# Kernel optimization log

Measured on AMD Instinct MI355X. Metric: run time of the kernel, lower is better.

The kernel has to match this reference:

```python
import jax, jax.numpy as jnp
import numpy as np

N = 50000      # nodes
E = 800000     # edges (before self-loops)
IN = 128       # in_channels
C = 64         # hidden_channels
HD = 4         # heads
SLOPE = 0.2    # GATConv leaky_relu negative slope
EPS_BN = 1e-5


def add_self_loops(edge_index, n):
    loop = jnp.arange(n, dtype=edge_index.dtype)
    return jnp.concatenate([edge_index, jnp.stack([loop, loop])], axis=1)


def gat_conv(x, edge_index, W, a_src, a_dst, bias, heads, out_c, concat, n):
    src, dst = edge_index[0], edge_index[1]
    h = (x @ W).reshape(n, heads, out_c)                 # [N,H,C]
    al_s = jnp.sum(h * a_src, axis=-1)                   # [N,H]
    al_d = jnp.sum(h * a_dst, axis=-1)                   # [N,H]
    e = jax.nn.leaky_relu(al_s[src] + al_d[dst], SLOPE)  # [Etot,H]
    m = jax.ops.segment_max(e, dst, num_segments=n)      # segment softmax (stable)
    ex = jnp.exp(e - m[dst])
    s = jax.ops.segment_sum(ex, dst, num_segments=n)
    alpha = ex / (s[dst] + 1e-16)                        # [Etot,H]
    out = jax.ops.segment_sum(h[src] * alpha[:, :, None], dst, num_segments=n)
    out = out.reshape(n, heads * out_c) if concat else out.mean(axis=1)
    return out + bias


def batch_norm(x, gamma, beta):
    mu = x.mean(axis=0)
    var = x.var(axis=0)
    return (x - mu) * jax.lax.rsqrt(var + EPS_BN) * gamma + beta


def setup_inputs() -> dict:
    key = jax.random.key(0)
    ks = jax.random.split(key, 24)
    f = lambda k, shp, sc: (jax.random.normal(k, shp, dtype=jnp.float32) * sc)
    HC = HD * C
    return {
        "x": f(ks[0], (N, IN), 1.0),
        "edge_index": jax.random.randint(ks[1], (2, E), 0, N, dtype=jnp.int64),
        # conv1: IN -> C, heads=HD, concat
        "W1": f(ks[2], (IN, HC), 0.05), "as1": f(ks[3], (HD, C), 0.05),
        "ad1": f(ks[4], (HD, C), 0.05), "b1": f(ks[5], (HC,), 0.02),
        "g1": jnp.ones((HC,), jnp.float32), "bb1": jnp.zeros((HC,), jnp.float32),
        # conv2: HC -> C, heads=HD, concat
        "W2": f(ks[6], (HC, HC), 0.05), "as2": f(ks[7], (HD, C), 0.05),
        "ad2": f(ks[8], (HD, C), 0.05), "b2": f(ks[9], (HC,), 0.02),
        "g2": jnp.ones((HC,), jnp.float32), "bb2": jnp.zeros((HC,), jnp.float32),
        # conv3: HC -> C, heads=1, mean
        "W3": f(ks[10], (HC, C), 0.05), "as3": f(ks[11], (1, C), 0.05),
        "ad3": f(ks[12], (1, C), 0.05), "b3": f(ks[13], (C,), 0.02),
        # skips
        "Ws1": f(ks[14], (IN, HC), 0.05), "bs1": f(ks[15], (HC,), 0.02),
        "Ws2": f(ks[16], (HC, C), 0.05), "bs2": f(ks[17], (C,), 0.02),
    }


def reference(x, edge_index, W1, as1, ad1, b1, g1, bb1,
              W2, as2, ad2, b2, g2, bb2,
              W3, as3, ad3, b3, Ws1, bs1, Ws2, bs2):
    ei = add_self_loops(edge_index, N)
    x_init = x @ Ws1 + bs1
    h = gat_conv(x, ei, W1, as1, ad1, b1, HD, C, True, N)
    h = jax.nn.elu(batch_norm(h, g1, bb1)) + x_init
    x_skip = h @ Ws2 + bs2
    h = gat_conv(h, ei, W2, as2, ad2, b2, HD, C, True, N)
    h = jax.nn.elu(batch_norm(h, g2, bb2))
    out = gat_conv(h, ei, W3, as3, ad3, b3, 1, C, False, N) + x_skip
    return out
```

## Files before the change

kernel.cpp:

```cpp
#include <hip/hip_runtime.h>
#include <hip/hip_bf16.h>
#include <cstdint>
#include <cstddef>


#define LRELU_SLOPE 0.2f

typedef __attribute__((ext_vector_type(8))) short short8;
typedef __attribute__((ext_vector_type(4))) float f32x4;

__device__ __forceinline__ float bf2f(unsigned short u) {
  union { unsigned int i; float f; } t; t.i = ((unsigned int)u) << 16; return t.f;
}
__device__ __forceinline__ unsigned short f2bf(float f) {
  __hip_bfloat16 h = __float2bfloat16(f);
  return *reinterpret_cast<unsigned short*>(&h);
}

template<int K, int WAVES_GAT, int WAVES_SKIP>
__global__ __launch_bounds__((WAVES_GAT + WAVES_SKIP) * 64)
void gemm_gat_fused(const unsigned short* __restrict__ A,
                    const unsigned short* __restrict__ BtH,
                    const unsigned short* __restrict__ BtS,
                    const float* __restrict__ a_s, const float* __restrict__ a_d,
                    const float* __restrict__ biasS,
                    unsigned short* __restrict__ Hout,
                    float* __restrict__ als, float* __restrict__ ald,
                    unsigned short* __restrict__ Sout, int M) {
  constexpr int NKS = K / 32;
  constexpr int NH  = WAVES_GAT * 64;
  constexpr int NS  = WAVES_SKIP * 64;
  const int wid  = threadIdx.x >> 6;
  const int lane = threadIdx.x & 63;
  const int r    = lane & 15;
  const int q    = lane >> 4;
  const int koff = q * 8;
  const bool isGat = wid < WAVES_GAT;
  const int colbase = isGat ? wid * 64 : (wid - WAVES_GAT) * 64;
  const unsigned short* Bt = isGat ? BtH : BtS;

  short8 b[4][NKS];
  #pragma unroll
  for (int nf = 0; nf < 4; ++nf)
    #pragma unroll
    for (int ks = 0; ks < NKS; ++ks)
      b[nf][ks] = *(const short8*)(Bt + (size_t)(colbase + nf * 16 + r) * K + ks * 32 + koff);

  float as4[4] = {}, ad4[4] = {};
  if (isGat) {
    #pragma unroll
    for (int nf = 0; nf < 4; ++nf) {
      as4[nf] = a_s[colbase + nf * 16 + r];
      ad4[nf] = a_d[colbase + nf * 16 + r];
    }
  }

  const int ntiles = (M + 15) >> 4;
  const int chunk = (ntiles + 7) >> 3;
  const int xcd   = blockIdx.x & 7;
  const int lo    = xcd * chunk;
  const int hi    = min(lo + chunk, ntiles);
  const int bstep = gridDim.x >> 3;
  for (int t = lo + (blockIdx.x >> 3); t < hi; t += bstep) {
    const int row = t * 16 + r;
    short8 a[NKS];
    #pragma unroll
    for (int ks = 0; ks < NKS; ++ks) {
      a[ks] = (short8)(short)0;
      if (row < M) a[ks] = *(const short8*)(A + (size_t)row * K + ks * 32 + koff);
    }
    f32x4 acc[4];
    #pragma unroll
    for (int nf = 0; nf < 4; ++nf) acc[nf] = (f32x4)0.0f;
    #pragma unroll
    for (int ks = 0; ks < NKS; ++ks)
      #pragma unroll
      for (int nf = 0; nf < 4; ++nf)
        acc[nf] = __builtin_amdgcn_mfma_f32_16x16x32_bf16(a[ks], b[nf][ks], acc[nf], 0, 0, 0);

    const int rbase = t * 16 + q * 4;
    if (isGat) {
      #pragma unroll
      for (int nf = 0; nf < 4; ++nf) {
        const int col = colbase + nf * 16 + r;
        #pragma unroll
        for (int i = 0; i < 4; ++i) {
          const int rr = rbase + i;
          if (rr < M) Hout[(size_t)rr * NH + col] = f2bf(acc[nf][i]);
        }
      }
      #pragma unroll
      for (int i = 0; i < 4; ++i) {
        float s = 0.f, d = 0.f;
        #pragma unroll
        for (int nf = 0; nf < 4; ++nf) {
          s = fmaf(acc[nf][i], as4[nf], s);
          d = fmaf(acc[nf][i], ad4[nf], d);
        }
        #pragma unroll
        for (int m = 8; m >= 1; m >>= 1) {
          s += __shfl_xor(s, m, 64);
          d += __shfl_xor(d, m, 64);
        }
        const int rr = rbase + i;
        if (r == 0 && rr < M) {
          als[(size_t)rr * WAVES_GAT + wid] = s;
          ald[(size_t)rr * WAVES_GAT + wid] = d;
        }
      }
    } else {
      #pragma unroll
      for (int nf = 0; nf < 4; ++nf) {
        const int col = colbase + nf * 16 + r;
        const float bs = biasS[col];
        #pragma unroll
        for (int i = 0; i < 4; ++i) {
          const int rr = rbase + i;
          if (rr < M) Sout[(size_t)rr * NS + col] = f2bf(acc[nf][i] + bs);
        }
      }
    }
  }
}

__global__ __launch_bounds__(256)
void gemm_gat3(const unsigned short* __restrict__ A, const unsigned short* __restrict__ Bt,
               const float* __restrict__ a_s, const float* __restrict__ a_d,
               unsigned short* __restrict__ Hout, float* __restrict__ als,
               float* __restrict__ ald, int M) {
  constexpr int K = 256, NKS = 8;
  const int wid  = threadIdx.x >> 6;
  const int lane = threadIdx.x & 63;
  const int r    = lane & 15;
  const int q    = lane >> 4;
  const int koff = q * 8;

  short8 b[4][NKS];
  #pragma unroll
  for (int nf = 0; nf < 4; ++nf)
    #pragma unroll
    for (int ks = 0; ks < NKS; ++ks)
      b[nf][ks] = *(const short8*)(Bt + (size_t)(nf * 16 + r) * K + ks * 32 + koff);
  float as4[4], ad4[4];
  #pragma unroll
  for (int nf = 0; nf < 4; ++nf) {
    as4[nf] = a_s[nf * 16 + r];
    ad4[nf] = a_d[nf * 16 + r];
  }

  const int ntiles = (M + 15) >> 4;
  const int chunk = (ntiles + 7) >> 3;
  const int xcd   = blockIdx.x & 7;
  const int lo    = xcd * chunk;
  const int hi    = min(lo + chunk, ntiles);
  const int bstep = (gridDim.x >> 3) * 4;
  for (int t = lo + (blockIdx.x >> 3) * 4 + wid; t < hi; t += bstep) {
    const int row = t * 16 + r;
    short8 a[NKS];
    #pragma unroll
    for (int ks = 0; ks < NKS; ++ks) {
      a[ks] = (short8)(short)0;
      if (row < M) a[ks] = *(const short8*)(A + (size_t)row * K + ks * 32 + koff);
    }
    f32x4 acc[4];
    #pragma unroll
    for (int nf = 0; nf < 4; ++nf) acc[nf] = (f32x4)0.0f;
    #pragma unroll
    for (int ks = 0; ks < NKS; ++ks)
      #pragma unroll
      for (int nf = 0; nf < 4; ++nf)
        acc[nf] = __builtin_amdgcn_mfma_f32_16x16x32_bf16(a[ks], b[nf][ks], acc[nf], 0, 0, 0);

    const int rbase = t * 16 + q * 4;
    #pragma unroll
    for (int nf = 0; nf < 4; ++nf) {
      const int col = nf * 16 + r;
      #pragma unroll
      for (int i = 0; i < 4; ++i) {
        const int rr = rbase + i;
        if (rr < M) Hout[(size_t)rr * 64 + col] = f2bf(acc[nf][i]);
      }
    }
    #pragma unroll
    for (int i = 0; i < 4; ++i) {
      float s = 0.f, d = 0.f;
      #pragma unroll
      for (int nf = 0; nf < 4; ++nf) {
        s = fmaf(acc[nf][i], as4[nf], s);
        d = fmaf(acc[nf][i], ad4[nf], d);
      }
      #pragma unroll
      for (int m = 8; m >= 1; m >>= 1) {
        s += __shfl_xor(s, m, 64);
        d += __shfl_xor(d, m, 64);
      }
      const int rr = rbase + i;
      if (r == 0 && rr < M) { als[rr] = s; ald[rr] = d; }
    }
  }
}

__global__ __launch_bounds__(256)
void prep_all(const float* __restrict__ x,
              const float* __restrict__ W1, const float* __restrict__ Ws1,
              const float* __restrict__ W2, const float* __restrict__ Ws2,
              const float* __restrict__ W3,
              unsigned short* __restrict__ xb,
              unsigned short* __restrict__ W1t, unsigned short* __restrict__ Ws1t,
              unsigned short* __restrict__ W2t, unsigned short* __restrict__ Ws2t,
              unsigned short* __restrict__ W3t, int n) {
  int idx = blockIdx.x * blockDim.x + threadIdx.x;
  const int nx = n * 32;
  if (idx < nx) {
    float4 v = ((const float4*)x)[idx];
    ushort4 o;
    o.x = f2bf(v.x); o.y = f2bf(v.y); o.z = f2bf(v.z); o.w = f2bf(v.w);
    ((ushort4*)xb)[idx] = o;
    return;
  }
  idx -= nx;
  if (idx < 256 * 128) { int nn = idx >> 7, kk = idx & 127; W1t[idx]  = f2bf(W1[kk * 256 + nn]);  return; }
  idx -= 256 * 128;
  if (idx < 256 * 128) { int nn = idx >> 7, kk = idx & 127; Ws1t[idx] = f2bf(Ws1[kk * 256 + nn]); return; }
  idx -= 256 * 128;
  if (idx < 256 * 256) { int nn = idx >> 8, kk = idx & 255; W2t[idx]  = f2bf(W2[kk * 256 + nn]);  return; }
  idx -= 256 * 256;
  if (idx < 64 * 256)  { int nn = idx >> 8, kk = idx & 255; Ws2t[idx] = f2bf(Ws2[kk * 64 + nn]);  return; }
  idx -= 64 * 256;
  if (idx < 64 * 256)  { int nn = idx >> 8, kk = idx & 255; W3t[idx]  = f2bf(W3[kk * 64 + nn]); }
}

__global__ void count_edges(const int* __restrict__ ei, int E, int* __restrict__ counts,
                            int n) {
  const int g = blockIdx.x & 7;
  const int chunk = (n + 7) >> 3;
  const int lo = g * chunk, hi = min(lo + chunk, n);
  const int stride = (gridDim.x >> 3) * blockDim.x;
  for (int i = (blockIdx.x >> 3) * blockDim.x + threadIdx.x; i < E; i += stride) {
    int d = ei[E + i];
    if (d >= lo && d < hi) atomicAdd(&counts[d], 1);
  }
}
__global__ void scan_block(const int* __restrict__ in, int* __restrict__ out,
                           int* __restrict__ bsums, int n) {
  __shared__ int tmp[256];
  int t = threadIdx.x;
  int gid = blockIdx.x * 256 + t;
  int v = (gid < n) ? in[gid] : 0;
  tmp[t] = v;
  __syncthreads();
  #pragma unroll
  for (int off = 1; off < 256; off <<= 1) {
    int x = (t >= off) ? tmp[t - off] : 0;
    __syncthreads();
    tmp[t] += x;
    __syncthreads();
  }
  if (gid < n) out[gid] = tmp[t] - v;
  if (t == 255) bsums[blockIdx.x] = tmp[255];
}
__global__ void scan_tops(const int* __restrict__ bsums, int* __restrict__ boffs, int nb) {
  __shared__ int tmp[256];
  int t = threadIdx.x;
  int v = (t < nb) ? bsums[t] : 0;
  tmp[t] = v;
  __syncthreads();
  #pragma unroll
  for (int off = 1; off < 256; off <<= 1) {
    int x = (t >= off) ? tmp[t - off] : 0;
    __syncthreads();
    tmp[t] += x;
    __syncthreads();
  }
  if (t < nb) boffs[t] = tmp[t] - v;
}
__global__ void scan_add(int* __restrict__ rp, const int* __restrict__ boffs,
                         int n, int etot) {
  int gid = blockIdx.x * 256 + threadIdx.x;
  if (gid < n) rp[gid] += boffs[blockIdx.x];
  if (gid == 0) rp[n] = etot;
}
__global__ void fill_edges(const int* __restrict__ ei, int E, const int* __restrict__ rp,
                           int* __restrict__ cursor, int* __restrict__ csr, int n) {
  const int g = blockIdx.x & 7;
  const int chunk = (n + 7) >> 3;
  const int lo = g * chunk, hi = min(lo + chunk, n);
  const int stride = (gridDim.x >> 3) * blockDim.x;
  for (int i = (blockIdx.x >> 3) * blockDim.x + threadIdx.x; i < E; i += stride) {
    int d = ei[E + i];
    if (d >= lo && d < hi) {
      int pos = rp[d] + atomicAdd(&cursor[d], 1);
      csr[pos] = ei[i];
    }
  }
}

template<int HEADS, int HCt, bool OUT_BF16>
__global__ __launch_bounds__(256)
void gat_aggregate(const unsigned short* __restrict__ H, const float* __restrict__ als,
                   const float* __restrict__ ald, const int* __restrict__ rp,
                   const int* __restrict__ csr, const float* __restrict__ bias,
                   const unsigned short* __restrict__ skip, void* __restrict__ out, int n) {
  constexpr int CPL = HCt / 64;
  int w = (blockIdx.x * blockDim.x + threadIdx.x) >> 6;
  int lane = threadIdx.x & 63;
  if (w >= n) return;
  const int beg = rp[w], end = rp[w + 1];
  const int myhead = (HEADS == 1) ? 0 : (lane >> 4);
  const float adh = ald[(size_t)w * HEADS + myhead];

  auto att = [&](int s) -> float {
    float e = als[(size_t)s * HEADS + myhead] + adh;
    e = fmaxf(e, LRELU_SLOPE * e);
    return __expf(e);
  };

  float acc[CPL];
  float ssum = att(w);
  {
    const unsigned short* hp = H + (size_t)w * HCt + lane * CPL;
    if constexpr (CPL == 4) {
      ushort4 hv = *(const ushort4*)hp;
      acc[0] = ssum * bf2f(hv.x); acc[1] = ssum * bf2f(hv.y);
      acc[2] = ssum * bf2f(hv.z); acc[3] = ssum * bf2f(hv.w);
    } else {
      acc[0] = ssum * bf2f(hp[0]);
    }
  }

  int j = beg;
  for (; j + 8 <= end; j += 8) {
    int sidx[8];
    #pragma unroll
    for (int u = 0; u < 8; ++u) sidx[u] = csr[j + u];
    if constexpr (CPL == 4) {
      ushort4 hv[8];
      #pragma unroll
      for (int u = 0; u < 8; ++u)
        hv[u] = *(const ushort4*)(H + (size_t)sidx[u] * HCt + lane * 4);
      float ex[8];
      #pragma unroll
      for (int u = 0; u < 8; ++u) ex[u] = att(sidx[u]);
      #pragma unroll
      for (int u = 0; u < 8; ++u) {
        ssum += ex[u];
        acc[0] = fmaf(ex[u], bf2f(hv[u].x), acc[0]);
        acc[1] = fmaf(ex[u], bf2f(hv[u].y), acc[1]);
        acc[2] = fmaf(ex[u], bf2f(hv[u].z), acc[2]);
        acc[3] = fmaf(ex[u], bf2f(hv[u].w), acc[3]);
      }
    } else {
      unsigned short hv[8];
      #pragma unroll
      for (int u = 0; u < 8; ++u) hv[u] = H[(size_t)sidx[u] * HCt + lane];
      float ex[8];
      #pragma unroll
      for (int u = 0; u < 8; ++u) ex[u] = att(sidx[u]);
      #pragma unroll
      for (int u = 0; u < 8; ++u) {
        ssum += ex[u];
        acc[0] = fmaf(ex[u], bf2f(hv[u]), acc[0]);
      }
    }
  }
  for (; j + 4 <= end; j += 4) {
    int sidx[4];
    #pragma unroll
    for (int u = 0; u < 4; ++u) sidx[u] = csr[j + u];
    float ex[4];
    #pragma unroll
    for (int u = 0; u < 4; ++u) ex[u] = att(sidx[u]);
    if constexpr (CPL == 4) {
      ushort4 hv[4];
      #pragma unroll
      for (int u = 0; u < 4; ++u)
        hv[u] = *(const ushort4*)(H + (size_t)sidx[u] * HCt + lane * 4);
      #pragma unroll
      for (int u = 0; u < 4; ++u) {
        ssum += ex[u];
        acc[0] = fmaf(ex[u], bf2f(hv[u].x), acc[0]);
        acc[1] = fmaf(ex[u], bf2f(hv[u].y), acc[1]);
        acc[2] = fmaf(ex[u], bf2f(hv[u].z), acc[2]);
        acc[3] = fmaf(ex[u], bf2f(hv[u].w), acc[3]);
      }
    } else {
      unsigned short hv[4];
      #pragma unroll
      for (int u = 0; u < 4; ++u) hv[u] = H[(size_t)sidx[u] * HCt + lane];
      #pragma unroll
      for (int u = 0; u < 4; ++u) {
        ssum += ex[u];
        acc[0] = fmaf(ex[u], bf2f(hv[u]), acc[0]);
      }
    }
  }
  for (; j < end; ++j) {
    const int s = csr[j];
    const float ex = att(s);
    ssum += ex;
    const unsigned short* hp = H + (size_t)s * HCt + lane * CPL;
    if constexpr (CPL == 4) {
      ushort4 hv = *(const ushort4*)hp;
      acc[0] = fmaf(ex, bf2f(hv.x), acc[0]);
      acc[1] = fmaf(ex, bf2f(hv.y), acc[1]);
      acc[2] = fmaf(ex, bf2f(hv.z), acc[2]);
      acc[3] = fmaf(ex, bf2f(hv.w), acc[3]);
    } else {
      acc[0] = fmaf(ex, bf2f(hp[0]), acc[0]);
    }
  }

  const float inv = 1.f / (ssum + 1e-16f);
  #pragma unroll
  for (int c = 0; c < CPL; ++c) {
    int ch = lane * CPL + c;
    float v = acc[c] * inv + bias[ch];
    if (skip) v += bf2f(skip[(size_t)w * HCt + ch]);
    if constexpr (OUT_BF16)
      ((unsigned short*)out)[(size_t)w * HCt + ch] = f2bf(v);
    else
      ((float*)out)[(size_t)w * HCt + ch] = v;
  }
}

__global__ __launch_bounds__(256)
void bn_stats(const unsigned short* __restrict__ X, float* __restrict__ sums, int n) {
  int c = threadIdx.x;
  float s = 0.f, q = 0.f;
  for (int r = blockIdx.x; r < n; r += gridDim.x) {
    float v = bf2f(X[(size_t)r * 256 + c]);
    s += v;
    q = fmaf(v, v, q);
  }
  atomicAdd(&sums[c], s);
  atomicAdd(&sums[256 + c], q);
}
__global__ void bn_finalize(const float* __restrict__ sums, const float* __restrict__ gamma,
                            const float* __restrict__ beta, float* __restrict__ scsh,
                            int n) {
  int c = threadIdx.x;
  if (c < 256) {
    float mean = sums[c] / (float)n;
    float var = sums[256 + c] / (float)n - mean * mean;
    float sc = gamma[c] * rsqrtf(var + 1e-5f);
    scsh[c] = sc;
    scsh[256 + c] = beta[c] - mean * sc;
  }
}
__global__ __launch_bounds__(256)
void bn_apply_elu(const unsigned short* __restrict__ X, const float* __restrict__ scsh,
                  const unsigned short* __restrict__ skip, unsigned short* __restrict__ Y,
                  int total) {
  int i4 = blockIdx.x * blockDim.x + threadIdx.x;
  if (i4 * 4 >= total) return;
  ushort4 xv = ((const ushort4*)X)[i4];
  int cb = (i4 * 4) & 255;
  float4 sc = *(const float4*)(scsh + cb);
  float4 sh = *(const float4*)(scsh + 256 + cb);
  float4 y;
  y.x = fmaf(bf2f(xv.x), sc.x, sh.x);
  y.y = fmaf(bf2f(xv.y), sc.y, sh.y);
  y.z = fmaf(bf2f(xv.z), sc.z, sh.z);
  y.w = fmaf(bf2f(xv.w), sc.w, sh.w);
  y.x = (y.x > 0.f) ? y.x : expm1f(y.x);
  y.y = (y.y > 0.f) ? y.y : expm1f(y.y);
  y.z = (y.z > 0.f) ? y.z : expm1f(y.z);
  y.w = (y.w > 0.f) ? y.w : expm1f(y.w);
  if (skip) {
    ushort4 s4 = ((const ushort4*)skip)[i4];
    y.x += bf2f(s4.x); y.y += bf2f(s4.y); y.z += bf2f(s4.z); y.w += bf2f(s4.w);
  }
  ushort4 o;
  o.x = f2bf(y.x); o.y = f2bf(y.y); o.z = f2bf(y.z); o.w = f2bf(y.w);
  ((ushort4*)Y)[i4] = o;
}

extern "C" void kernel_launch(void* const* d_in, const int* in_sizes, int n_in,
                              void* d_out, int out_size, void* d_ws, size_t ws_size,
                              hipStream_t stream) {
  const float* x   = (const float*)d_in[0];
  const int*   ei  = (const int*)d_in[1];
  const float* W1  = (const float*)d_in[2];
  const float* as1 = (const float*)d_in[3];
  const float* ad1 = (const float*)d_in[4];
  const float* b1  = (const float*)d_in[5];
  const float* g1  = (const float*)d_in[6];
  const float* bb1 = (const float*)d_in[7];
  const float* W2  = (const float*)d_in[8];
  const float* as2 = (const float*)d_in[9];
  const float* ad2 = (const float*)d_in[10];
  const float* b2  = (const float*)d_in[11];
  const float* g2  = (const float*)d_in[12];
  const float* bb2 = (const float*)d_in[13];
  const float* W3  = (const float*)d_in[14];
  const float* as3 = (const float*)d_in[15];
  const float* ad3 = (const float*)d_in[16];
  const float* b3  = (const float*)d_in[17];
  const float* Ws1 = (const float*)d_in[18];
  const float* bs1 = (const float*)d_in[19];
  const float* Ws2 = (const float*)d_in[20];
  const float* bs2 = (const float*)d_in[21];

  const int n = in_sizes[0] / 128;
  const int E = in_sizes[1] / 2;

  char* wsp = (char*)d_ws;
  auto carve = [&](size_t bytes) -> void* {
    void* p = (void*)wsp;
    wsp += (bytes + 255) & ~(size_t)255;
    return p;
  };
  unsigned short* Hb  = (unsigned short*)carve((size_t)n * 256 * 2);
  unsigned short* hb  = (unsigned short*)carve((size_t)n * 256 * 2);
  unsigned short* xbD = (unsigned short*)carve((size_t)n * 128 * 2);
  unsigned short* xb  = xbD;
  unsigned short* D   = xbD;
  unsigned short* Bv  = (unsigned short*)carve((size_t)n * 256 * 2);
  unsigned short* Cv  = (unsigned short*)carve((size_t)n * 256 * 2);
  float* als  = (float*)carve((size_t)n * 4 * 4);
  float* ald  = (float*)carve((size_t)n * 4 * 4);
  int*   rp   = (int*)carve((size_t)(n + 1) * 4);
  int*   cnt  = (int*)carve((size_t)n * 4);
  int*   bsums= (int*)carve(256 * 4);
  int*   boffs= (int*)carve(256 * 4);
  int*   csr  = (int*)carve((size_t)E * 4);
  float* bnb  = (float*)carve(4 * 256 * 4);
  float* sums = bnb;
  float* scsh = bnb + 512;
  unsigned short* W1t  = (unsigned short*)carve(128 * 256 * 2);
  unsigned short* Ws1t = (unsigned short*)carve(128 * 256 * 2);
  unsigned short* W2t  = (unsigned short*)carve(256 * 256 * 2);
  unsigned short* Ws2t = (unsigned short*)carve(256 * 64 * 2);
  unsigned short* W3t  = (unsigned short*)carve(256 * 64 * 2);

  const int NB = (n + 255) / 256;

  hipMemsetAsync(cnt, 0, (size_t)n * 4, stream);
  count_edges<<<2048, 256, 0, stream>>>(ei, E, cnt, n);
  scan_block<<<NB, 256, 0, stream>>>(cnt, rp, bsums, n);
  scan_tops<<<1, 256, 0, stream>>>(bsums, boffs, NB);
  scan_add<<<NB, 256, 0, stream>>>(rp, boffs, n, E);
  hipMemsetAsync(cnt, 0, (size_t)n * 4, stream);
  fill_edges<<<2048, 256, 0, stream>>>(ei, E, rp, cnt, csr, n);

  {
    const int total = n * 32 + 2 * 256 * 128 + 256 * 256 + 2 * 64 * 256;
    prep_all<<<(total + 255) / 256, 256, 0, stream>>>(x, W1, Ws1, W2, Ws2, W3,
                                                      xb, W1t, Ws1t, W2t, Ws2t, W3t, n);
  }

  const int wgrid = (n * 64 + 255) / 256;
  const int egrid = (n * 256 / 4 + 255) / 256;

  gemm_gat_fused<128, 4, 4><<<512, 512, 0, stream>>>(
      xb, W1t, Ws1t, as1, ad1, bs1, Hb, als, ald, Bv, n);
  gat_aggregate<4, 256, true><<<wgrid, 256, 0, stream>>>(Hb, als, ald, rp, csr, b1,
                                                         nullptr, Cv, n);
  hipMemsetAsync(sums, 0, 512 * 4, stream);
  bn_stats<<<256, 256, 0, stream>>>(Cv, sums, n);
  bn_finalize<<<1, 256, 0, stream>>>(sums, g1, bb1, scsh, n);
  bn_apply_elu<<<egrid, 256, 0, stream>>>(Cv, scsh, Bv, hb, n * 256);

  gemm_gat_fused<256, 4, 1><<<512, 320, 0, stream>>>(
      hb, W2t, Ws2t, as2, ad2, bs2, Hb, als, ald, D, n);
  gat_aggregate<4, 256, true><<<wgrid, 256, 0, stream>>>(Hb, als, ald, rp, csr, b2,
                                                         nullptr, Cv, n);
  hipMemsetAsync(sums, 0, 512 * 4, stream);
  bn_stats<<<256, 256, 0, stream>>>(Cv, sums, n);
  bn_finalize<<<1, 256, 0, stream>>>(sums, g2, bb2, scsh, n);
  bn_apply_elu<<<egrid, 256, 0, stream>>>(Cv, scsh, nullptr, hb, n * 256);

  gemm_gat3<<<512, 256, 0, stream>>>(hb, W3t, as3, ad3, Hb, als, ald, n);
  gat_aggregate<1, 64, false><<<wgrid, 256, 0, stream>>>(Hb, als, ald, rp, csr, b3, D,
                                                         d_out, n);
}
```

Measured before the change: 513.2 us.

## Fuse batch-norm statistics into GAT aggregation and share attention exps via shuffles

The per-column sum and sum-of-squares for batch norm are now accumulated inside the aggregation kernel. Each block reduces them through shared-memory atomics and then adds into global sums, which removes the separate bn_stats pass that re-read the activations, plus two memsets. Zeroing of the sums moves into prep_all and bn_finalize. The aggregation kernel becomes a persistent grid-stride loop over nodes. In the 8-edge loop, each lane computes one attention exp and broadcasts it with shuffles, instead of every lane computing all eight. The trade-offs are more atomic traffic at block end, stats taken from fp32 values before bf16 rounding, and a fixed grid size of 2048 blocks.

```diff
diff --git a/kernel.cpp b/kernel.cpp
--- a/kernel.cpp
+++ b/kernel.cpp
@@ -208,7 +208,7 @@
               unsigned short* __restrict__ xb,
               unsigned short* __restrict__ W1t, unsigned short* __restrict__ Ws1t,
               unsigned short* __restrict__ W2t, unsigned short* __restrict__ Ws2t,
-              unsigned short* __restrict__ W3t, int n) {
+              unsigned short* __restrict__ W3t, float* __restrict__ sums, int n) {
   int idx = blockIdx.x * blockDim.x + threadIdx.x;
   const int nx = n * 32;
   if (idx < nx) {
@@ -227,7 +227,9 @@
   idx -= 256 * 256;
   if (idx < 64 * 256)  { int nn = idx >> 8, kk = idx & 255; Ws2t[idx] = f2bf(Ws2[kk * 64 + nn]);  return; }
   idx -= 64 * 256;
-  if (idx < 64 * 256)  { int nn = idx >> 8, kk = idx & 255; W3t[idx]  = f2bf(W3[kk * 64 + nn]); }
+  if (idx < 64 * 256)  { int nn = idx >> 8, kk = idx & 255; W3t[idx]  = f2bf(W3[kk * 64 + nn]); return; }
+  idx -= 64 * 256;
+  if (idx < 512) sums[idx] = 0.f;
 }
 
 __global__ void count_edges(const int* __restrict__ ei, int E, int* __restrict__ counts,
@@ -295,147 +297,162 @@
   }
 }
 
-template<int HEADS, int HCt, bool OUT_BF16>
+template<int HEADS, int HCt, bool OUT_BF16, bool STATS>
 __global__ __launch_bounds__(256)
 void gat_aggregate(const unsigned short* __restrict__ H, const float* __restrict__ als,
                    const float* __restrict__ ald, const int* __restrict__ rp,
                    const int* __restrict__ csr, const float* __restrict__ bias,
-                   const unsigned short* __restrict__ skip, void* __restrict__ out, int n) {
+                   const unsigned short* __restrict__ skip, void* __restrict__ out,
+                   float* __restrict__ sums, int n) {
   constexpr int CPL = HCt / 64;
-  int w = (blockIdx.x * blockDim.x + threadIdx.x) >> 6;
-  int lane = threadIdx.x & 63;
-  if (w >= n) return;
-  const int beg = rp[w], end = rp[w + 1];
+  const int wid  = threadIdx.x >> 6;
+  const int lane = threadIdx.x & 63;
   const int myhead = (HEADS == 1) ? 0 : (lane >> 4);
-  const float adh = ald[(size_t)w * HEADS + myhead];
-
-  auto att = [&](int s) -> float {
-    float e = als[(size_t)s * HEADS + myhead] + adh;
-    e = fmaxf(e, LRELU_SLOPE * e);
-    return __expf(e);
-  };
-
-  float acc[CPL];
-  float ssum = att(w);
-  {
-    const unsigned short* hp = H + (size_t)w * HCt + lane * CPL;
-    if constexpr (CPL == 4) {
-      ushort4 hv = *(const ushort4*)hp;
-      acc[0] = ssum * bf2f(hv.x); acc[1] = ssum * bf2f(hv.y);
-      acc[2] = ssum * bf2f(hv.z); acc[3] = ssum * bf2f(hv.w);
-    } else {
-      acc[0] = ssum * bf2f(hp[0]);
-    }
-  }
-
-  int j = beg;
-  for (; j + 8 <= end; j += 8) {
-    int sidx[8];
-    #pragma unroll
-    for (int u = 0; u < 8; ++u) sidx[u] = csr[j + u];
-    if constexpr (CPL == 4) {
-      ushort4 hv[8];
-      #pragma unroll
-      for (int u = 0; u < 8; ++u)
-        hv[u] = *(const ushort4*)(H + (size_t)sidx[u] * HCt + lane * 4);
+  const int gw0 = blockIdx.x * 4 + wid;
+  const int nw  = gridDim.x * 4;
+  float ls[CPL] = {}, lq[CPL] = {};
+
+  for (int w = gw0; w < n; w += nw) {
+    const int beg = rp[w], end = rp[w + 1];
+    const float adh = ald[(size_t)w * HEADS + myhead];
+
+    auto att = [&](int s) -> float {
+      float e = als[(size_t)s * HEADS + myhead] + adh;
+      e = fmaxf(e, LRELU_SLOPE * e);
+      return __expf(e);
+    };
+
+    float acc[CPL];
+    float ssum = att(w);
+    {
+      const unsigned short* hp = H + (size_t)w * HCt + lane * CPL;
+      if constexpr (CPL == 4) {
+        ushort4 hv = *(const ushort4*)hp;
+        acc[0] = ssum * bf2f(hv.x); acc[1] = ssum * bf2f(hv.y);
+        acc[2] = ssum * bf2f(hv.z); acc[3] = ssum * bf2f(hv.w);
+      } else {
+        acc[0] = ssum * bf2f(hp[0]);
+      }
+    }
+
+    int j = beg;
+    for (; j + 8 <= end; j += 8) {
+      int sidx[8];
+      #pragma unroll
+      for (int u = 0; u < 8; ++u) sidx[u] = csr[j + u];
+      const int myS = csr[j + (lane & 7)];
+      float e = als[(size_t)myS * HEADS + myhead] + adh;
+      e = fmaxf(e, LRELU_SLOPE * e);
+      e = __expf(e);
       float ex[8];
       #pragma unroll
-      for (int u = 0; u < 8; ++u) ex[u] = att(sidx[u]);
-      #pragma unroll
-      for (int u = 0; u < 8; ++u) {
-        ssum += ex[u];
-        acc[0] = fmaf(ex[u], bf2f(hv[u].x), acc[0]);
-        acc[1] = fmaf(ex[u], bf2f(hv[u].y), acc[1]);
-        acc[2] = fmaf(ex[u], bf2f(hv[u].z), acc[2]);
-        acc[3] = fmaf(ex[u], bf2f(hv[u].w), acc[3]);
-      }
-    } else {
-      unsigned short hv[8];
-      #pragma unroll
-      for (int u = 0; u < 8; ++u) hv[u] = H[(size_t)sidx[u] * HCt + lane];
-      float ex[8];
-      #pragma unroll
-      for (int u = 0; u < 8; ++u) ex[u] = att(sidx[u]);
-      #pragma unroll
-      for (int u = 0; u < 8; ++u) {
-        ssum += ex[u];
-        acc[0] = fmaf(ex[u], bf2f(hv[u]), acc[0]);
-      }
-    }
-  }
-  for (; j + 4 <= end; j += 4) {
-    int sidx[4];
-    #pragma unroll
-    for (int u = 0; u < 4; ++u) sidx[u] = csr[j + u];
-    float ex[4];
-    #pragma unroll
-    for (int u = 0; u < 4; ++u) ex[u] = att(sidx[u]);
-    if constexpr (CPL == 4) {
-      ushort4 hv[4];
-      #pragma unroll
-      for (int u = 0; u < 4; ++u)
-        hv[u] = *(const ushort4*)(H + (size_t)sidx[u] * HCt + lane * 4);
-      #pragma unroll
-      for (int u = 0; u < 4; ++u) {
-        ssum += ex[u];
-        acc[0] = fmaf(ex[u], bf2f(hv[u].x), acc[0]);
-        acc[1] = fmaf(ex[u], bf2f(hv[u].y), acc[1]);
-        acc[2] = fmaf(ex[u], bf2f(hv[u].z), acc[2]);
-        acc[3] = fmaf(ex[u], bf2f(hv[u].w), acc[3]);
-      }
-    } else {
-      unsigned short hv[4];
-      #pragma unroll
-      for (int u = 0; u < 4; ++u) hv[u] = H[(size_t)sidx[u] * HCt + lane];
-      #pragma unroll
-      for (int u = 0; u < 4; ++u) {
-        ssum += ex[u];
-        acc[0] = fmaf(ex[u], bf2f(hv[u]), acc[0]);
-      }
-    }
-  }
-  for (; j < end; ++j) {
-    const int s = csr[j];
-    const float ex = att(s);
-    ssum += ex;
-    const unsigned short* hp = H + (size_t)s * HCt + lane * CPL;
-    if constexpr (CPL == 4) {
-      ushort4 hv = *(const ushort4*)hp;
-      acc[0] = fmaf(ex, bf2f(hv.x), acc[0]);
-      acc[1] = fmaf(ex, bf2f(hv.y), acc[1]);
-      acc[2] = fmaf(ex, bf2f(hv.z), acc[2]);
-      acc[3] = fmaf(ex, bf2f(hv.w), acc[3]);
-    } else {
-      acc[0] = fmaf(ex, bf2f(hp[0]), acc[0]);
-    }
-  }
-
-  const float inv = 1.f / (ssum + 1e-16f);
-  #pragma unroll
-  for (int c = 0; c < CPL; ++c) {
-    int ch = lane * CPL + c;
-    float v = acc[c] * inv + bias[ch];
-    if (skip) v += bf2f(skip[(size_t)w * HCt + ch]);
-    if constexpr (OUT_BF16)
-      ((unsigned short*)out)[(size_t)w * HCt + ch] = f2bf(v);
-    else
-      ((float*)out)[(size_t)w * HCt + ch] = v;
-  }
-}
-
-__global__ __launch_bounds__(256)
-void bn_stats(const unsigned short* __restrict__ X, float* __restrict__ sums, int n) {
-  int c = threadIdx.x;
-  float s = 0.f, q = 0.f;
-  for (int r = blockIdx.x; r < n; r += gridDim.x) {
-    float v = bf2f(X[(size_t)r * 256 + c]);
-    s += v;
-    q = fmaf(v, v, q);
-  }
-  atomicAdd(&sums[c], s);
-  atomicAdd(&sums[256 + c], q);
-}
-__global__ void bn_finalize(const float* __restrict__ sums, const float* __restrict__ gamma,
+      for (int u = 0; u < 8; ++u) ex[u] = __shfl(e, (lane & 48) | u, 64);
+      if constexpr (CPL == 4) {
+        ushort4 hv[8];
+        #pragma unroll
+        for (int u = 0; u < 8; ++u)
+          hv[u] = *(const ushort4*)(H + (size_t)sidx[u] * HCt + lane * 4);
+        #pragma unroll
+        for (int u = 0; u < 8; ++u) {
+          ssum += ex[u];
+          acc[0] = fmaf(ex[u], bf2f(hv[u].x), acc[0]);
+          acc[1] = fmaf(ex[u], bf2f(hv[u].y), acc[1]);
+          acc[2] = fmaf(ex[u], bf2f(hv[u].z), acc[2]);
+          acc[3] = fmaf(ex[u], bf2f(hv[u].w), acc[3]);
+        }
+      } else {
+        unsigned short hv[8];
+        #pragma unroll
+        for (int u = 0; u < 8; ++u) hv[u] = H[(size_t)sidx[u] * HCt + lane];
+        #pragma unroll
+        for (int u = 0; u < 8; ++u) {
+          ssum += ex[u];
+          acc[0] = fmaf(ex[u], bf2f(hv[u]), acc[0]);
+        }
+      }
+    }
+    for (; j + 4 <= end; j += 4) {
+      int sidx[4];
+      #pragma unroll
+      for (int u = 0; u < 4; ++u) sidx[u] = csr[j + u];
+      float ex[4];
+      #pragma unroll
+      for (int u = 0; u < 4; ++u) ex[u] = att(sidx[u]);
+      if constexpr (CPL == 4) {
+        ushort4 hv[4];
+        #pragma unroll
+        for (int u = 0; u < 4; ++u)
+          hv[u] = *(const ushort4*)(H + (size_t)sidx[u] * HCt + lane * 4);
+        #pragma unroll
+        for (int u = 0; u < 4; ++u) {
+          ssum += ex[u];
+          acc[0] = fmaf(ex[u], bf2f(hv[u].x), acc[0]);
+          acc[1] = fmaf(ex[u], bf2f(hv[u].y), acc[1]);
+          acc[2] = fmaf(ex[u], bf2f(hv[u].z), acc[2]);
+          acc[3] = fmaf(ex[u], bf2f(hv[u].w), acc[3]);
+        }
+      } else {
+        unsigned short hv[4];
+        #pragma unroll
+        for (int u = 0; u < 4; ++u) hv[u] = H[(size_t)sidx[u] * HCt + lane];
+        #pragma unroll
+        for (int u = 0; u < 4; ++u) {
+          ssum += ex[u];
+          acc[0] = fmaf(ex[u], bf2f(hv[u]), acc[0]);
+        }
+      }
+    }
+    for (; j < end; ++j) {
+      const int s = csr[j];
+      const float ex = att(s);
+      ssum += ex;
+      const unsigned short* hp = H + (size_t)s * HCt + lane * CPL;
+      if constexpr (CPL == 4) {
+        ushort4 hv = *(const ushort4*)hp;
+        acc[0] = fmaf(ex, bf2f(hv.x), acc[0]);
+        acc[1] = fmaf(ex, bf2f(hv.y), acc[1]);
+        acc[2] = fmaf(ex, bf2f(hv.z), acc[2]);
+        acc[3] = fmaf(ex, bf2f(hv.w), acc[3]);
+      } else {
+        acc[0] = fmaf(ex, bf2f(hp[0]), acc[0]);
+      }
+    }
+
+    const float inv = 1.f / (ssum + 1e-16f);
+    #pragma unroll
+    for (int c = 0; c < CPL; ++c) {
+      int ch = lane * CPL + c;
+      float v = acc[c] * inv + bias[ch];
+      if (skip) v += bf2f(skip[(size_t)w * HCt + ch]);
+      if constexpr (STATS) {
+        ls[c] += v;
+        lq[c] = fmaf(v, v, lq[c]);
+      }
+      if constexpr (OUT_BF16)
+        ((unsigned short*)out)[(size_t)w * HCt + ch] = f2bf(v);
+      else
+        ((float*)out)[(size_t)w * HCt + ch] = v;
+    }
+  }
+
+  if constexpr (STATS) {
+    __shared__ float red[512];
+    if (threadIdx.x < 256) { red[threadIdx.x] = 0.f; red[256 + threadIdx.x] = 0.f; }
+    __syncthreads();
+    #pragma unroll
+    for (int c = 0; c < CPL; ++c) {
+      atomicAdd(&red[lane * CPL + c], ls[c]);
+      atomicAdd(&red[256 + lane * CPL + c], lq[c]);
+    }
+    __syncthreads();
+    if (threadIdx.x < 256) {
+      atomicAdd(&sums[threadIdx.x], red[threadIdx.x]);
+      atomicAdd(&sums[256 + threadIdx.x], red[256 + threadIdx.x]);
+    }
+  }
+}
+
+__global__ void bn_finalize(float* __restrict__ sums, const float* __restrict__ gamma,
                             const float* __restrict__ beta, float* __restrict__ scsh,
                             int n) {
   int c = threadIdx.x;
@@ -445,6 +462,8 @@
     float sc = gamma[c] * rsqrtf(var + 1e-5f);
     scsh[c] = sc;
     scsh[256 + c] = beta[c] - mean * sc;
+    sums[c] = 0.f;
+    sums[256 + c] = 0.f;
   }
 }
 __global__ __launch_bounds__(256)
@@ -544,33 +563,30 @@
   fill_edges<<<2048, 256, 0, stream>>>(ei, E, rp, cnt, csr, n);
 
   {
-    const int total = n * 32 + 2 * 256 * 128 + 256 * 256 + 2 * 64 * 256;
+    const int total = n * 32 + 2 * 256 * 128 + 256 * 256 + 2 * 64 * 256 + 512;
     prep_all<<<(total + 255) / 256, 256, 0, stream>>>(x, W1, Ws1, W2, Ws2, W3,
-                                                      xb, W1t, Ws1t, W2t, Ws2t, W3t, n);
-  }
-
-  const int wgrid = (n * 64 + 255) / 256;
+                                                      xb, W1t, Ws1t, W2t, Ws2t, W3t,
+                                                      sums, n);
+  }
+
+  const int agrid = 2048;
   const int egrid = (n * 256 / 4 + 255) / 256;
 
   gemm_gat_fused<128, 4, 4><<<512, 512, 0, stream>>>(
       xb, W1t, Ws1t, as1, ad1, bs1, Hb, als, ald, Bv, n);
-  gat_aggregate<4, 256, true><<<wgrid, 256, 0, stream>>>(Hb, als, ald, rp, csr, b1,
-                                                         nullptr, Cv, n);
-  hipMemsetAsync(sums, 0, 512 * 4, stream);
-  bn_stats<<<256, 256, 0, stream>>>(Cv, sums, n);
+  gat_aggregate<4, 256, true, true><<<agrid, 256, 0, stream>>>(
+      Hb, als, ald, rp, csr, b1, nullptr, Cv, sums, n);
   bn_finalize<<<1, 256, 0, stream>>>(sums, g1, bb1, scsh, n);
   bn_apply_elu<<<egrid, 256, 0, stream>>>(Cv, scsh, Bv, hb, n * 256);
 
   gemm_gat_fused<256, 4, 1><<<512, 320, 0, stream>>>(
       hb, W2t, Ws2t, as2, ad2, bs2, Hb, als, ald, D, n);
-  gat_aggregate<4, 256, true><<<wgrid, 256, 0, stream>>>(Hb, als, ald, rp, csr, b2,
-                                                         nullptr, Cv, n);
-  hipMemsetAsync(sums, 0, 512 * 4, stream);
-  bn_stats<<<256, 256, 0, stream>>>(Cv, sums, n);
+  gat_aggregate<4, 256, true, true><<<agrid, 256, 0, stream>>>(
+      Hb, als, ald, rp, csr, b2, nullptr, Cv, sums, n);
   bn_finalize<<<1, 256, 0, stream>>>(sums, g2, bb2, scsh, n);
   bn_apply_elu<<<egrid, 256, 0, stream>>>(Cv, scsh, nullptr, hb, n * 256);
 
   gemm_gat3<<<512, 256, 0, stream>>>(hb, W3t, as3, ad3, Hb, als, ald, n);
-  gat_aggregate<1, 64, false><<<wgrid, 256, 0, stream>>>(Hb, als, ald, rp, csr, b3, D,
-                                                         d_out, n);
-}
+  gat_aggregate<1, 64, false, false><<<agrid, 256, 0, stream>>>(
+      Hb, als, ald, rp, csr, b3, D, d_out, nullptr, n);
+}
```

Measured after the change: 489.7 us. -4.6%, faster.
